# Kernel optimization log

Measured on AMD Instinct MI355X. Metric: run time of the kernel, lower is better.

The kernel has to match this reference:

```python
import jax, jax.numpy as jnp
import numpy as np
from jax.scipy.special import logsumexp

S = 4          # num_residual_streams
D = 1024       # dim
B, T = 2, 4096
SINKHORN_ITERS = 10
TAU = 0.05


def rmsnorm(x, gamma):
    # F.normalize(x, dim=-1) * sqrt(dim) * (gamma + 1)
    norm = jnp.sqrt(jnp.sum(x * x, axis=-1, keepdims=True))
    scale = jnp.asarray(x.shape[-1], x.dtype) ** 0.5
    return x / jnp.maximum(norm, 1e-12) * scale * (gamma + 1.0)


def sinkhorn_log(logits, num_iters=SINKHORN_ITERS, tau=TAU):
    Z = logits / tau                      # (..., n, n)
    u = jnp.zeros(Z.shape[:-1], Z.dtype)  # (..., n)
    v = jnp.zeros_like(u)
    for _ in range(num_iters):
        u = -logsumexp(Z + v[..., None, :], axis=-1)
        v = -logsumexp(Z + u[..., :, None], axis=-2)
    return jnp.exp(Z + u[..., :, None] + v[..., None, :])


def setup_inputs() -> dict:
    key = jax.random.key(0)
    ks = jax.random.split(key, 8)
    residuals = jax.random.normal(ks[0], (B, T, S, D), dtype=jnp.float32)
    gamma = jnp.zeros((S * D,), dtype=jnp.float32)             # RMSNorm gamma init
    w_res = 0.02 * jax.random.normal(ks[1], (S * S, S * D), dtype=jnp.float32)
    w_pre = 0.02 * jax.random.normal(ks[2], (S, S * D), dtype=jnp.float32)
    w_post = 0.02 * jax.random.normal(ks[3], (S, S * D), dtype=jnp.float32)
    beta_res = jnp.full((S, S), -8.0, dtype=jnp.float32).at[jnp.arange(S), jnp.arange(S)].set(0.0)
    beta_pre = jnp.full((S,), -8.0, dtype=jnp.float32).at[0].set(0.0)  # layer_index=0
    beta_post = jnp.zeros((S,), dtype=jnp.float32)
    alpha_res = jnp.asarray(0.01, dtype=jnp.float32)
    alpha_pre = jnp.asarray(0.01, dtype=jnp.float32)
    alpha_post = jnp.asarray(0.01, dtype=jnp.float32)
    return dict(residuals=residuals, gamma=gamma, w_res=w_res, w_pre=w_pre,
                w_post=w_post, beta_res=beta_res, beta_pre=beta_pre,
                beta_post=beta_post, alpha_res=alpha_res, alpha_pre=alpha_pre,
                alpha_post=alpha_post)


def reference(residuals, gamma, w_res, w_pre, w_post, beta_res, beta_pre,
              beta_post, alpha_res, alpha_pre, alpha_post):
    b, t, s, d = residuals.shape
    h = residuals.reshape(b, t, s * d)
    normed = rmsnorm(h, gamma)                                  # (b,t,s*d)
    # dynamic H logits: static beta + alpha * linear(normed)
    res_logits = beta_res + alpha_res * jnp.einsum('btk,ek->bte', normed, w_res).reshape(b, t, s, s)
    H_res = sinkhorn_log(res_logits)                            # (b,t,s,s) doubly stochastic
    H_pre = jax.nn.softmax(beta_pre + alpha_pre * jnp.einsum('btk,sk->bts', normed, w_pre), axis=-1)
    H_post = 2.0 * jax.nn.sigmoid(beta_post + alpha_post * jnp.einsum('btk,sk->bts', normed, w_post))
    branch_in = jnp.einsum('bts,btsd->btd', H_pre, residuals)   # stream pooling -> branch input
    branch_out = branch_in                                      # identity branch
    mixed = jnp.einsum('btij,btjd->btid', H_res, residuals)     # stream remixing
    out = mixed + H_post[..., None] * branch_out[:, :, None, :]
    return out
```

## Files before the change

kernel.cpp:

```cpp
#include <hip/hip_runtime.h>
#include <hip/hip_bf16.h>
#include <math.h>

#define TOK_PER_BLK 4
#define THREADS 256
#define CHUNK 2
#define NCHUNK 12
#define NROWS 24
#define PCOL 68
#define TAU_INV 20.0f

__global__ __launch_bounds__(THREADS, 3)
void hc_fused(const float* __restrict__ resid,
              const float* __restrict__ gamma,
              const float* __restrict__ w_res,
              const float* __restrict__ w_pre,
              const float* __restrict__ w_post,
              const float* __restrict__ beta_res,
              const float* __restrict__ beta_pre,
              const float* __restrict__ beta_post,
              const float* __restrict__ p_alpha_res,
              const float* __restrict__ p_alpha_pre,
              const float* __restrict__ p_alpha_post,
              float* __restrict__ out)
{
    __shared__ float sh_part[NROWS * TOK_PER_BLK][PCOL];
    __shared__ float sh_ssqp[TOK_PER_BLK][PCOL];
    __shared__ float sh_raw[TOK_PER_BLK][NROWS];
    __shared__ float sh_ssq[TOK_PER_BLK];
    __shared__ float sh_H[TOK_PER_BLK][NROWS];

    const int tid  = threadIdx.x;
    const int wave = tid >> 6;
    const int lane = tid & 63;
    const long tok0 = (long)blockIdx.x * TOK_PER_BLK;

    const float4* hp = (const float4*)resid + tok0 * 1024;
    float4 p[TOK_PER_BLK][4];
    #pragma unroll
    for (int m = 0; m < TOK_PER_BLK; ++m) {
        #pragma unroll
        for (int q = 0; q < 4; ++q)
            p[m][q] = hp[m * 1024 + q * 256 + tid];
    }
    #pragma unroll
    for (int m = 0; m < TOK_PER_BLK; ++m) {
        float s = 0.f;
        #pragma unroll
        for (int q = 0; q < 4; ++q) {
            float4 v = p[m][q];
            s += v.x * v.x + v.y * v.y + v.z * v.z + v.w * v.w;
        }
        s += __shfl_xor(s, 16, 64);
        s += __shfl_xor(s, 32, 64);
        if (lane < 16) sh_ssqp[m][wave * 16 + lane] = s;
    }

    float4 g[4];
    {
        const float4* gp = (const float4*)gamma;
        #pragma unroll
        for (int q = 0; q < 4; ++q) {
            float4 gv = gp[q * 256 + tid];
            g[q] = make_float4(gv.x + 1.f, gv.y + 1.f, gv.z + 1.f, gv.w + 1.f);
        }
    }

    auto load_chunk = [&](int c, float4 (&w)[CHUNK][4]) {
        #pragma unroll
        for (int r = 0; r < CHUNK; ++r) {
            const int e = c * CHUNK + r;
            const float* wr = (e < 16) ? (w_res + (size_t)e * 4096)
                            : (e < 20) ? (w_pre + (size_t)(e - 16) * 4096)
                                       : (w_post + (size_t)(e - 20) * 4096);
            const float4* wr4 = (const float4*)wr;
            #pragma unroll
            for (int q = 0; q < 4; ++q) w[r][q] = wr4[q * 256 + tid];
        }
    };
    auto compute_chunk = [&](int c, const float4 (&w)[CHUNK][4]) {
        #pragma unroll
        for (int r = 0; r < CHUNK; ++r) {
            float4 wg[4];
            #pragma unroll
            for (int q = 0; q < 4; ++q)
                wg[q] = make_float4(w[r][q].x * g[q].x, w[r][q].y * g[q].y,
                                    w[r][q].z * g[q].z, w[r][q].w * g[q].w);
            #pragma unroll
            for (int m = 0; m < TOK_PER_BLK; ++m) {
                float a = 0.f;
                #pragma unroll
                for (int q = 0; q < 4; ++q)
                    a += wg[q].x * p[m][q].x + wg[q].y * p[m][q].y
                       + wg[q].z * p[m][q].z + wg[q].w * p[m][q].w;
                a += __shfl_xor(a, 16, 64);
                a += __shfl_xor(a, 32, 64);
                if (lane < 16)
                    sh_part[(c * CHUNK + r) * TOK_PER_BLK + m][wave * 16 + lane] = a;
            }
        }
    };

    float4 wA[CHUNK][4], wB[CHUNK][4];
    load_chunk(0, wA);
    #pragma unroll 1
    for (int cc = 0; cc < NCHUNK / 2; ++cc) {
        load_chunk(2 * cc + 1, wB);
        compute_chunk(2 * cc, wA);
        if (cc + 1 < NCHUNK / 2) load_chunk(2 * cc + 2, wA);
        compute_chunk(2 * cc + 1, wB);
    }
    __syncthreads();

    if (tid < NROWS * TOK_PER_BLK) {
        const int e = tid >> 2, m = tid & 3;
        const float4* src = (const float4*)&sh_part[e * TOK_PER_BLK + m][0];
        float4 s4 = src[0];
        #pragma unroll
        for (int j = 1; j < 16; ++j) {
            float4 v = src[j];
            s4.x += v.x; s4.y += v.y; s4.z += v.z; s4.w += v.w;
        }
        sh_raw[m][e] = s4.x + s4.y + s4.z + s4.w;
    } else if (tid < NROWS * TOK_PER_BLK + TOK_PER_BLK) {
        const int m = tid - NROWS * TOK_PER_BLK;
        const float4* src = (const float4*)&sh_ssqp[m][0];
        float4 s4 = src[0];
        #pragma unroll
        for (int j = 1; j < 16; ++j) {
            float4 v = src[j];
            s4.x += v.x; s4.y += v.y; s4.z += v.z; s4.w += v.w;
        }
        sh_ssq[m] = s4.x + s4.y + s4.z + s4.w;
    }
    __syncthreads();

    {
        const int m   = wave;
        const int idx = lane & 15;
        const int jj  = idx & 3;

        float ss    = sh_ssq[m];
        float scale = 64.0f / fmaxf(sqrtf(ss), 1e-12f);

        const float a_res  = p_alpha_res[0];
        const float a_pre  = p_alpha_pre[0];
        const float a_post = p_alpha_post[0];

        float Z = (beta_res[idx] + a_res * scale * sh_raw[m][idx]) * TAU_INV;
        float u = 0.f, v = 0.f;
        #pragma unroll 1
        for (int it = 0; it < 10; ++it) {
            float t  = Z + v;
            float mx = t;
            mx = fmaxf(mx, __shfl_xor(mx, 1, 64));
            mx = fmaxf(mx, __shfl_xor(mx, 2, 64));
            float sm = __expf(t - mx);
            sm += __shfl_xor(sm, 1, 64);
            sm += __shfl_xor(sm, 2, 64);
            u = -(mx + __logf(sm));
            t  = Z + u;
            mx = t;
            mx = fmaxf(mx, __shfl_xor(mx, 4, 64));
            mx = fmaxf(mx, __shfl_xor(mx, 8, 64));
            sm = __expf(t - mx);
            sm += __shfl_xor(sm, 4, 64);
            sm += __shfl_xor(sm, 8, 64);
            v = -(mx + __logf(sm));
        }
        float P = __expf(Z + u + v);
        if (lane < 16) sh_H[m][idx] = P;

        float lpre = beta_pre[jj] + a_pre * scale * sh_raw[m][16 + jj];
        float mxp = lpre;
        mxp = fmaxf(mxp, __shfl_xor(mxp, 1, 64));
        mxp = fmaxf(mxp, __shfl_xor(mxp, 2, 64));
        float ep = __expf(lpre - mxp);
        float sp = ep;
        sp += __shfl_xor(sp, 1, 64);
        sp += __shfl_xor(sp, 2, 64);
        float hpre = ep / sp;
        float lpost = beta_post[jj] + a_post * scale * sh_raw[m][20 + jj];
        float hpost = 2.0f / (1.0f + __expf(-lpost));
        if (lane < 4) { sh_H[m][16 + jj] = hpre; sh_H[m][20 + jj] = hpost; }
    }
    __syncthreads();

    #pragma unroll
    for (int m = 0; m < TOK_PER_BLK; ++m) {
        float Hr[16], Hp[4], Ho[4];
        #pragma unroll
        for (int k = 0; k < 16; ++k) Hr[k] = sh_H[m][k];
        #pragma unroll
        for (int s = 0; s < 4; ++s) { Hp[s] = sh_H[m][16 + s]; Ho[s] = sh_H[m][20 + s]; }

        float4 br;
        br.x = Hp[0]*p[m][0].x + Hp[1]*p[m][1].x + Hp[2]*p[m][2].x + Hp[3]*p[m][3].x;
        br.y = Hp[0]*p[m][0].y + Hp[1]*p[m][1].y + Hp[2]*p[m][2].y + Hp[3]*p[m][3].y;
        br.z = Hp[0]*p[m][0].z + Hp[1]*p[m][1].z + Hp[2]*p[m][2].z + Hp[3]*p[m][3].z;
        br.w = Hp[0]*p[m][0].w + Hp[1]*p[m][1].w + Hp[2]*p[m][2].w + Hp[3]*p[m][3].w;

        float4* op = (float4*)out + (tok0 + m) * 1024;
        #pragma unroll
        for (int i = 0; i < 4; ++i) {
            float4 o;
            o.x = Hr[i*4+0]*p[m][0].x + Hr[i*4+1]*p[m][1].x + Hr[i*4+2]*p[m][2].x + Hr[i*4+3]*p[m][3].x + Ho[i]*br.x;
            o.y = Hr[i*4+0]*p[m][0].y + Hr[i*4+1]*p[m][1].y + Hr[i*4+2]*p[m][2].y + Hr[i*4+3]*p[m][3].y + Ho[i]*br.y;
            o.z = Hr[i*4+0]*p[m][0].z + Hr[i*4+1]*p[m][1].z + Hr[i*4+2]*p[m][2].z + Hr[i*4+3]*p[m][3].z + Ho[i]*br.z;
            o.w = Hr[i*4+0]*p[m][0].w + Hr[i*4+1]*p[m][1].w + Hr[i*4+2]*p[m][2].w + Hr[i*4+3]*p[m][3].w + Ho[i]*br.w;
            op[i * 256 + tid] = o;
        }
    }
}

extern "C" void kernel_launch(void* const* d_in, const int* in_sizes, int n_in,
                              void* d_out, int out_size, void* d_ws, size_t ws_size,
                              hipStream_t stream) {
    const float* resid      = (const float*)d_in[0];
    const float* gamma      = (const float*)d_in[1];
    const float* w_res      = (const float*)d_in[2];
    const float* w_pre      = (const float*)d_in[3];
    const float* w_post     = (const float*)d_in[4];
    const float* beta_res   = (const float*)d_in[5];
    const float* beta_pre   = (const float*)d_in[6];
    const float* beta_post  = (const float*)d_in[7];
    const float* alpha_res  = (const float*)d_in[8];
    const float* alpha_pre  = (const float*)d_in[9];
    const float* alpha_post = (const float*)d_in[10];
    float* out = (float*)d_out;

    const int ntok = in_sizes[0] / 4096;
    const int grid = ntok / TOK_PER_BLK;

    hc_fused<<<grid, THREADS, 0, stream>>>(resid, gamma, w_res, w_pre, w_post,
                                           beta_res, beta_pre, beta_post,
                                           alpha_res, alpha_pre, alpha_post, out);
}
```

Before: 305.7 us.

## Stream weight rows into LDS via async global_load_lds double buffering

Weight rows for the 24 projection outputs are now copied asynchronously into a double-buffered LDS tile with global_load_lds, instead of being loaded into registers in chunks. Each row is consumed from LDS under barriers, with explicit vmcnt waits to overlap the next row's fetch. Two extra shuffle steps shrink each wave's partials to 4 values, so the partial buffers drop to 17 columns, and the lower register use allows raising the occupancy hint to 4 blocks. The cost is about 32KB more LDS per block and two barriers per row, and the hand-written vmcnt counts must stay correct.

```diff
diff --git a/kernel.cpp b/kernel.cpp
--- a/kernel.cpp
+++ b/kernel.cpp
@@ -1,16 +1,19 @@
 #include <hip/hip_runtime.h>
-#include <hip/hip_bf16.h>
 #include <math.h>
 
 #define TOK_PER_BLK 4
 #define THREADS 256
-#define CHUNK 2
-#define NCHUNK 12
 #define NROWS 24
-#define PCOL 68
+#define PCOL 17
 #define TAU_INV 20.0f
 
-__global__ __launch_bounds__(THREADS, 3)
+__device__ __forceinline__ void async_cp16(const float* gsrc, float* ldst) {
+    __builtin_amdgcn_global_load_lds(
+        (const __attribute__((address_space(1))) void*)gsrc,
+        (__attribute__((address_space(3))) void*)ldst, 16, 0, 0);
+}
+
+__global__ __launch_bounds__(THREADS, 4)
 void hc_fused(const float* __restrict__ resid,
               const float* __restrict__ gamma,
               const float* __restrict__ w_res,
@@ -24,6 +27,7 @@
               const float* __restrict__ p_alpha_post,
               float* __restrict__ out)
 {
+    __shared__ float sh_w[2][4096];
     __shared__ float sh_part[NROWS * TOK_PER_BLK][PCOL];
     __shared__ float sh_ssqp[TOK_PER_BLK][PCOL];
     __shared__ float sh_raw[TOK_PER_BLK][NROWS];
@@ -51,9 +55,11 @@
             float4 v = p[m][q];
             s += v.x * v.x + v.y * v.y + v.z * v.z + v.w * v.w;
         }
+        s += __shfl_xor(s, 4, 64);
+        s += __shfl_xor(s, 8, 64);
         s += __shfl_xor(s, 16, 64);
         s += __shfl_xor(s, 32, 64);
-        if (lane < 16) sh_ssqp[m][wave * 16 + lane] = s;
+        if (lane < 4) sh_ssqp[m][(wave << 2) | lane] = s;
     }
 
     float4 g[4];
@@ -66,72 +72,68 @@
         }
     }
 
-    auto load_chunk = [&](int c, float4 (&w)[CHUNK][4]) {
-        #pragma unroll
-        for (int r = 0; r < CHUNK; ++r) {
-            const int e = c * CHUNK + r;
-            const float* wr = (e < 16) ? (w_res + (size_t)e * 4096)
-                            : (e < 20) ? (w_pre + (size_t)(e - 16) * 4096)
-                                       : (w_post + (size_t)(e - 20) * 4096);
-            const float4* wr4 = (const float4*)wr;
-            #pragma unroll
-            for (int q = 0; q < 4; ++q) w[r][q] = wr4[q * 256 + tid];
-        }
+    auto row_ptr = [&](int e) -> const float* {
+        return (e < 16) ? (w_res + (size_t)e * 4096)
+             : (e < 20) ? (w_pre + (size_t)(e - 16) * 4096)
+                        : (w_post + (size_t)(e - 20) * 4096);
     };
-    auto compute_chunk = [&](int c, const float4 (&w)[CHUNK][4]) {
-        #pragma unroll
-        for (int r = 0; r < CHUNK; ++r) {
-            float4 wg[4];
-            #pragma unroll
-            for (int q = 0; q < 4; ++q)
-                wg[q] = make_float4(w[r][q].x * g[q].x, w[r][q].y * g[q].y,
-                                    w[r][q].z * g[q].z, w[r][q].w * g[q].w);
-            #pragma unroll
-            for (int m = 0; m < TOK_PER_BLK; ++m) {
-                float a = 0.f;
-                #pragma unroll
-                for (int q = 0; q < 4; ++q)
-                    a += wg[q].x * p[m][q].x + wg[q].y * p[m][q].y
-                       + wg[q].z * p[m][q].z + wg[q].w * p[m][q].w;
-                a += __shfl_xor(a, 16, 64);
-                a += __shfl_xor(a, 32, 64);
-                if (lane < 16)
-                    sh_part[(c * CHUNK + r) * TOK_PER_BLK + m][wave * 16 + lane] = a;
-            }
+    auto issue_row = [&](int e, int b) {
+        const float* src = row_ptr(e);
+        #pragma unroll
+        for (int j = 0; j < 4; ++j) {
+            const int seg = ((wave << 2) | j) << 8;
+            async_cp16(src + seg + (lane << 2), &sh_w[b][seg]);
         }
     };
 
-    float4 wA[CHUNK][4], wB[CHUNK][4];
-    load_chunk(0, wA);
+    issue_row(0, 0);
     #pragma unroll 1
-    for (int cc = 0; cc < NCHUNK / 2; ++cc) {
-        load_chunk(2 * cc + 1, wB);
-        compute_chunk(2 * cc, wA);
-        if (cc + 1 < NCHUNK / 2) load_chunk(2 * cc + 2, wA);
-        compute_chunk(2 * cc + 1, wB);
+    for (int r = 0; r < NROWS; ++r) {
+        const int b = r & 1;
+        if (r + 1 < NROWS) {
+            issue_row(r + 1, b ^ 1);
+            asm volatile("s_waitcnt vmcnt(4)" ::: "memory");
+        } else {
+            asm volatile("s_waitcnt vmcnt(0)" ::: "memory");
+        }
+        __builtin_amdgcn_s_barrier();
+        __builtin_amdgcn_sched_barrier(0);
+
+        const float4* wr = (const float4*)sh_w[b];
+        float4 w0 = wr[tid], w1 = wr[256 + tid], w2 = wr[512 + tid], w3 = wr[768 + tid];
+        w0 = make_float4(w0.x * g[0].x, w0.y * g[0].y, w0.z * g[0].z, w0.w * g[0].w);
+        w1 = make_float4(w1.x * g[1].x, w1.y * g[1].y, w1.z * g[1].z, w1.w * g[1].w);
+        w2 = make_float4(w2.x * g[2].x, w2.y * g[2].y, w2.z * g[2].z, w2.w * g[2].w);
+        w3 = make_float4(w3.x * g[3].x, w3.y * g[3].y, w3.z * g[3].z, w3.w * g[3].w);
+        #pragma unroll
+        for (int m = 0; m < TOK_PER_BLK; ++m) {
+            float a = w0.x * p[m][0].x + w0.y * p[m][0].y + w0.z * p[m][0].z + w0.w * p[m][0].w
+                    + w1.x * p[m][1].x + w1.y * p[m][1].y + w1.z * p[m][1].z + w1.w * p[m][1].w
+                    + w2.x * p[m][2].x + w2.y * p[m][2].y + w2.z * p[m][2].z + w2.w * p[m][2].w
+                    + w3.x * p[m][3].x + w3.y * p[m][3].y + w3.z * p[m][3].z + w3.w * p[m][3].w;
+            a += __shfl_xor(a, 4, 64);
+            a += __shfl_xor(a, 8, 64);
+            a += __shfl_xor(a, 16, 64);
+            a += __shfl_xor(a, 32, 64);
+            if (lane < 4) sh_part[r * TOK_PER_BLK + m][(wave << 2) | lane] = a;
+        }
+        __builtin_amdgcn_s_barrier();
     }
     __syncthreads();
 
     if (tid < NROWS * TOK_PER_BLK) {
         const int e = tid >> 2, m = tid & 3;
-        const float4* src = (const float4*)&sh_part[e * TOK_PER_BLK + m][0];
-        float4 s4 = src[0];
-        #pragma unroll
-        for (int j = 1; j < 16; ++j) {
-            float4 v = src[j];
-            s4.x += v.x; s4.y += v.y; s4.z += v.z; s4.w += v.w;
-        }
-        sh_raw[m][e] = s4.x + s4.y + s4.z + s4.w;
+        const float* src = &sh_part[tid][0];
+        float s = 0.f;
+        #pragma unroll
+        for (int j = 0; j < 16; ++j) s += src[j];
+        sh_raw[m][e] = s;
     } else if (tid < NROWS * TOK_PER_BLK + TOK_PER_BLK) {
         const int m = tid - NROWS * TOK_PER_BLK;
-        const float4* src = (const float4*)&sh_ssqp[m][0];
-        float4 s4 = src[0];
-        #pragma unroll
-        for (int j = 1; j < 16; ++j) {
-            float4 v = src[j];
-            s4.x += v.x; s4.y += v.y; s4.z += v.z; s4.w += v.w;
-        }
-        sh_ssq[m] = s4.x + s4.y + s4.z + s4.w;
+        float s = 0.f;
+        #pragma unroll
+        for (int j = 0; j < 16; ++j) s += sh_ssqp[m][j];
+        sh_ssq[m] = s;
     }
     __syncthreads();
 
```

Measured after the change: 329.9 us. 1.08x slower.

## Prefold gamma into weights in a prep kernel and raise occupancy

Applied to the files above, without the earlier changes.

Adds a small pre-kernel that multiplies the 24 weight rows by (1+gamma) once into workspace, so the main kernel no longer holds gamma in registers or rescales weights per token block. The main loop now double-buffers single weight rows instead of pairs, and launch bounds go from 3 to 4 blocks per SIMD. The intent is to free registers for higher occupancy and remove redundant multiplies, at the cost of an extra kernel launch and a small weight write and read through the workspace.

```diff
diff --git a/kernel.cpp b/kernel.cpp
--- a/kernel.cpp
+++ b/kernel.cpp
@@ -1,21 +1,28 @@
 #include <hip/hip_runtime.h>
-#include <hip/hip_bf16.h>
 #include <math.h>
 
 #define TOK_PER_BLK 4
 #define THREADS 256
-#define CHUNK 2
-#define NCHUNK 12
 #define NROWS 24
 #define PCOL 68
 #define TAU_INV 20.0f
 
-__global__ __launch_bounds__(THREADS, 3)
+__global__ void fold_gamma(const float* __restrict__ w_res,
+                           const float* __restrict__ w_pre,
+                           const float* __restrict__ w_post,
+                           const float* __restrict__ gamma,
+                           float* __restrict__ wf) {
+    const int idx = blockIdx.x * THREADS + threadIdx.x;
+    const int e = idx >> 12, k = idx & 4095;
+    const float* src = (e < 16) ? (w_res + ((size_t)e << 12))
+                     : (e < 20) ? (w_pre + ((size_t)(e - 16) << 12))
+                                : (w_post + ((size_t)(e - 20) << 12));
+    wf[idx] = src[k] * (1.0f + gamma[k]);
+}
+
+__global__ __launch_bounds__(THREADS, 4)
 void hc_fused(const float* __restrict__ resid,
-              const float* __restrict__ gamma,
-              const float* __restrict__ w_res,
-              const float* __restrict__ w_pre,
-              const float* __restrict__ w_post,
+              const float* __restrict__ wf,
               const float* __restrict__ beta_res,
               const float* __restrict__ beta_pre,
               const float* __restrict__ beta_post,
@@ -24,8 +31,8 @@
               const float* __restrict__ p_alpha_post,
               float* __restrict__ out)
 {
-    __shared__ float sh_part[NROWS * TOK_PER_BLK][PCOL];
-    __shared__ float sh_ssqp[TOK_PER_BLK][PCOL];
+    __shared__ __align__(16) float sh_part[NROWS * TOK_PER_BLK][PCOL];
+    __shared__ __align__(16) float sh_ssqp[TOK_PER_BLK][PCOL];
     __shared__ float sh_raw[TOK_PER_BLK][NROWS];
     __shared__ float sh_ssq[TOK_PER_BLK];
     __shared__ float sh_H[TOK_PER_BLK][NROWS];
@@ -56,59 +63,34 @@
         if (lane < 16) sh_ssqp[m][wave * 16 + lane] = s;
     }
 
-    float4 g[4];
-    {
-        const float4* gp = (const float4*)gamma;
-        #pragma unroll
-        for (int q = 0; q < 4; ++q) {
-            float4 gv = gp[q * 256 + tid];
-            g[q] = make_float4(gv.x + 1.f, gv.y + 1.f, gv.z + 1.f, gv.w + 1.f);
-        }
-    }
-
-    auto load_chunk = [&](int c, float4 (&w)[CHUNK][4]) {
-        #pragma unroll
-        for (int r = 0; r < CHUNK; ++r) {
-            const int e = c * CHUNK + r;
-            const float* wr = (e < 16) ? (w_res + (size_t)e * 4096)
-                            : (e < 20) ? (w_pre + (size_t)(e - 16) * 4096)
-                                       : (w_post + (size_t)(e - 20) * 4096);
-            const float4* wr4 = (const float4*)wr;
-            #pragma unroll
-            for (int q = 0; q < 4; ++q) w[r][q] = wr4[q * 256 + tid];
-        }
+    const float4* wp = (const float4*)wf;
+
+    auto load_row = [&](int e, float4 (&w)[4]) {
+        const float4* wr = wp + ((size_t)e << 10);
+        #pragma unroll
+        for (int q = 0; q < 4; ++q) w[q] = wr[q * 256 + tid];
     };
-    auto compute_chunk = [&](int c, const float4 (&w)[CHUNK][4]) {
-        #pragma unroll
-        for (int r = 0; r < CHUNK; ++r) {
-            float4 wg[4];
-            #pragma unroll
-            for (int q = 0; q < 4; ++q)
-                wg[q] = make_float4(w[r][q].x * g[q].x, w[r][q].y * g[q].y,
-                                    w[r][q].z * g[q].z, w[r][q].w * g[q].w);
-            #pragma unroll
-            for (int m = 0; m < TOK_PER_BLK; ++m) {
-                float a = 0.f;
-                #pragma unroll
-                for (int q = 0; q < 4; ++q)
-                    a += wg[q].x * p[m][q].x + wg[q].y * p[m][q].y
-                       + wg[q].z * p[m][q].z + wg[q].w * p[m][q].w;
-                a += __shfl_xor(a, 16, 64);
-                a += __shfl_xor(a, 32, 64);
-                if (lane < 16)
-                    sh_part[(c * CHUNK + r) * TOK_PER_BLK + m][wave * 16 + lane] = a;
-            }
+    auto comp_row = [&](int e, const float4 (&w)[4]) {
+        #pragma unroll
+        for (int m = 0; m < TOK_PER_BLK; ++m) {
+            float a = w[0].x * p[m][0].x + w[0].y * p[m][0].y + w[0].z * p[m][0].z + w[0].w * p[m][0].w
+                    + w[1].x * p[m][1].x + w[1].y * p[m][1].y + w[1].z * p[m][1].z + w[1].w * p[m][1].w
+                    + w[2].x * p[m][2].x + w[2].y * p[m][2].y + w[2].z * p[m][2].z + w[2].w * p[m][2].w
+                    + w[3].x * p[m][3].x + w[3].y * p[m][3].y + w[3].z * p[m][3].z + w[3].w * p[m][3].w;
+            a += __shfl_xor(a, 16, 64);
+            a += __shfl_xor(a, 32, 64);
+            if (lane < 16) sh_part[e * TOK_PER_BLK + m][wave * 16 + lane] = a;
         }
     };
 
-    float4 wA[CHUNK][4], wB[CHUNK][4];
-    load_chunk(0, wA);
+    float4 wA[4], wB[4];
+    load_row(0, wA);
     #pragma unroll 1
-    for (int cc = 0; cc < NCHUNK / 2; ++cc) {
-        load_chunk(2 * cc + 1, wB);
-        compute_chunk(2 * cc, wA);
-        if (cc + 1 < NCHUNK / 2) load_chunk(2 * cc + 2, wA);
-        compute_chunk(2 * cc + 1, wB);
+    for (int cc = 0; cc < 12; ++cc) {
+        load_row(2 * cc + 1, wB);
+        comp_row(2 * cc, wA);
+        if (cc < 11) load_row(2 * cc + 2, wA);
+        comp_row(2 * cc + 1, wB);
     }
     __syncthreads();
 
@@ -229,10 +211,16 @@
     const float* alpha_post = (const float*)d_in[10];
     float* out = (float*)d_out;
 
+    float* wf = (float*)d_ws;
+    (void)ws_size;
+
+    fold_gamma<<<NROWS * 4096 / THREADS, THREADS, 0, stream>>>(
+        w_res, w_pre, w_post, gamma, wf);
+
     const int ntok = in_sizes[0] / 4096;
     const int grid = ntok / TOK_PER_BLK;
 
-    hc_fused<<<grid, THREADS, 0, stream>>>(resid, gamma, w_res, w_pre, w_post,
-                                           beta_res, beta_pre, beta_post,
-                                           alpha_res, alpha_pre, alpha_post, out);
+    hc_fused<<<grid, THREADS, 0, stream>>>(resid, wf, beta_res, beta_pre,
+                                           beta_post, alpha_res, alpha_pre,
+                                           alpha_post, out);
 }
```

Result: slower. 352.5 us (+15.3%).
